# Kernel optimization log

Measured on AMD Instinct MI355X. Metric: run time of the kernel, lower is better.

## Reference

```python
import jax, jax.numpy as jnp
import numpy as np

N_USER, N_TX, E = 50000, 50000, 600000
D_USER, D_TX, D_ALIGN, HID, OUT = 128, 64, 128, 256, 128


def setup_inputs() -> dict:
    key = jax.random.key(0)
    ks = jax.random.split(key, 16)
    s = 0.05
    return {
        "x_user": jax.random.normal(ks[0], (N_USER, D_USER), jnp.float32),
        "x_tx": jax.random.normal(ks[1], (N_TX, D_TX), jnp.float32),
        "edge_user_tx": jax.random.randint(ks[2], (2, E), 0, N_USER),
        "edge_tx_user": jax.random.randint(ks[3], (2, E), 0, N_TX),
        "W_align_user": jax.random.normal(ks[4], (D_USER, D_ALIGN), jnp.float32) * s,
        "b_align_user": jnp.zeros((D_ALIGN,), jnp.float32),
        "W_align_tx": jax.random.normal(ks[5], (D_TX, D_ALIGN), jnp.float32) * s,
        "b_align_tx": jnp.zeros((D_ALIGN,), jnp.float32),
        "eps_ut": jnp.zeros((), jnp.float32),
        "eps_tu": jnp.zeros((), jnp.float32),
        "W1_ut": jax.random.normal(ks[6], (D_TX + D_ALIGN, HID), jnp.float32) * s,
        "b1_ut": jnp.zeros((HID,), jnp.float32),
        "W2_ut": jax.random.normal(ks[7], (HID, OUT), jnp.float32) * s,
        "b2_ut": jnp.zeros((OUT,), jnp.float32),
        "W1_tu": jax.random.normal(ks[8], (D_USER + D_ALIGN, HID), jnp.float32) * s,
        "b1_tu": jnp.zeros((HID,), jnp.float32),
        "W2_tu": jax.random.normal(ks[9], (HID, OUT), jnp.float32) * s,
        "b2_tu": jnp.zeros((OUT,), jnp.float32),
    }


def _mlp(h, W1, b1, W2, b2):
    return jnp.maximum(h @ W1 + b1, 0.0) @ W2 + b2


def _hexgin_conv(x_src, x_dst, edge_index, W_a, b_a, eps, W1, b1, W2, b2):
    # align src features, gather along edges, scatter-sum into dst nodes
    a_src = x_src @ W_a + b_a                       # [N_src, D_ALIGN]
    msgs = a_src[edge_index[0]]                     # [E, D_ALIGN] gather
    agg = jax.ops.segment_sum(msgs, edge_index[1], num_segments=x_dst.shape[0])
    h = jnp.concatenate([(1.0 + eps) * x_dst, agg], axis=1)
    return _mlp(h, W1, b1, W2, b2)


def reference(x_user, x_tx, edge_user_tx, edge_tx_user,
              W_align_user, b_align_user, W_align_tx, b_align_tx,
              eps_ut, eps_tu,
              W1_ut, b1_ut, W2_ut, b2_ut,
              W1_tu, b1_tu, W2_tu, b2_tu):
    # relation (user, makes, tx): updates tx nodes
    out_tx = _hexgin_conv(x_user, x_tx, edge_user_tx,
                          W_align_user, b_align_user, eps_ut,
                          W1_ut, b1_ut, W2_ut, b2_ut)
    # relation (tx, to, user): updates user nodes
    out_user = _hexgin_conv(x_tx, x_user, edge_tx_user,
                            W_align_tx, b_align_tx, eps_tu,
                            W1_tu, b1_tu, W2_tu, b2_tu)
    # HeteroConv aggr='sum': single relation per target, so plain outputs
    return out_user, out_tx
```

## Files before the change

kernel.cpp:

```cpp
#include <hip/hip_runtime.h>
#include <hip/hip_bf16.h>


#define D_USER 128
#define D_TX 64
#define D_ALIGN 128
#define HID 256
#define OUT_D 128
#define NNODE 50000
#define BI 32
#define MAXSLOT 62

typedef __attribute__((ext_vector_type(8))) short short8;
typedef __attribute__((ext_vector_type(4))) float f32x4;
typedef unsigned short ush;

__device__ __forceinline__ ush f2bf(float f) {
    union { float f; unsigned u; } v; v.f = f;
    unsigned u = v.u + 0x7fffu + ((v.u >> 16) & 1u);
    return (ush)(u >> 16);
}
__device__ __forceinline__ float2 bfu2f(unsigned u) {
    union { unsigned u; float f; } a, b;
    a.u = (u & 0xffffu) << 16;
    b.u = u & 0xffff0000u;
    return make_float2(a.f, b.f);
}
__device__ __forceinline__ unsigned f2bfu(float2 v) {
    return (unsigned)f2bf(v.x) | ((unsigned)f2bf(v.y) << 16);
}
__device__ __forceinline__ uint4 scale_bf8(uint4 v, float e) {
    unsigned* w = (unsigned*)&v;
    #pragma unroll
    for (int t = 0; t < 4; ++t) {
        float2 f = bfu2f(w[t]);
        w[t] = f2bfu(make_float2(f.x * e, f.y * e));
    }
    return v;
}

__global__ __launch_bounds__(256) void prep(
    const float* __restrict__ xu, ush* __restrict__ xbu,
    const float* __restrict__ xt, ush* __restrict__ xbt, int n8u, int n8t,
    const float* __restrict__ Wa_u, const float* __restrict__ ba_u,
    const float* __restrict__ W1_ut,
    const float* __restrict__ Wa_t, const float* __restrict__ ba_t,
    const float* __restrict__ W1_tu,
    const float* __restrict__ W2_ut, const float* __restrict__ W2_tu,
    ush* __restrict__ Bt1a, float* __restrict__ bfv1,
    ush* __restrict__ Bt1b, float* __restrict__ bfv2,
    ush* __restrict__ Bt2a, ush* __restrict__ Bt2b, int gb)
{
    int b = blockIdx.x, tid = threadIdx.x;
    if (b < gb) {
        int i = b * 256 + tid;
        const float* x; ush* xb; int j;
        if (i < n8u) { x = xu; xb = xbu; j = i; }
        else if (i < n8u + n8t) { x = xt; xb = xbt; j = i - n8u; }
        else return;
        const float4 a = *reinterpret_cast<const float4*>(&x[(size_t)j * 8]);
        const float4 c = *reinterpret_cast<const float4*>(&x[(size_t)j * 8 + 4]);
        ush o[8];
        o[0] = f2bf(a.x); o[1] = f2bf(a.y); o[2] = f2bf(a.z); o[3] = f2bf(a.w);
        o[4] = f2bf(c.x); o[5] = f2bf(c.y); o[6] = f2bf(c.z); o[7] = f2bf(c.w);
        *reinterpret_cast<uint4*>(&xb[(size_t)j * 8]) = *reinterpret_cast<uint4*>(o);
        return;
    }
    int idx = (b - gb) * 256 + tid;
    const int KT = 192;
    const int SEG1 = HID * (KT + 1);
    const int SEG2 = OUT_D * HID;
    if (idx < 2 * SEG1) {
        bool r2 = idx >= SEG1;
        int id = r2 ? idx - SEG1 : idx;
        const float* Wa = r2 ? Wa_t : Wa_u;
        const float* ba = r2 ? ba_t : ba_u;
        const float* W1 = r2 ? W1_tu : W1_ut;
        ush* Bt = r2 ? Bt1b : Bt1a;
        float* bfv = r2 ? bfv2 : bfv1;
        const int Dd = r2 ? 128 : 64;
        int c = id & (HID - 1);
        int k = id >> 8;
        const float* w1bot = W1 + (size_t)Dd * HID;
        if (k < Dd) {
            Bt[(size_t)c * KT + k] = f2bf(W1[(size_t)k * HID + c]);
        } else if (k < KT) {
            int ks = k - Dd;
            float acc = 0.f;
            for (int j = 0; j < D_ALIGN; ++j)
                acc += Wa[ks * D_ALIGN + j] * w1bot[(size_t)j * HID + c];
            Bt[(size_t)c * KT + k] = f2bf(acc);
        } else {
            float acc = 0.f;
            for (int j = 0; j < D_ALIGN; ++j)
                acc += ba[j] * w1bot[(size_t)j * HID + c];
            bfv[c] = acc;
        }
    } else if (idx < 2 * SEG1 + 2 * SEG2) {
        int id = idx - 2 * SEG1;
        bool r2 = id >= SEG2;
        if (r2) id -= SEG2;
        const float* W2 = r2 ? W2_tu : W2_ut;
        ush* Bt2 = r2 ? Bt2b : Bt2a;
        int c = id & (OUT_D - 1);
        int k = id >> 7;
        Bt2[(size_t)c * HID + k] = f2bf(W2[(size_t)k * OUT_D + c]);
    }
}

__global__ void fill_direct(const int* __restrict__ e_ut, const int* __restrict__ e_tu,
                            int E, int* __restrict__ pad)
{
    int i = blockIdx.x * blockDim.x + threadIdx.x;
    if (i >= 2 * E) return;
    int d, s;
    if (i < E) { d = e_ut[E + i];                    s = e_ut[i]; }
    else       { int j = i - E; d = NNODE + e_tu[E + j]; s = e_tu[j]; }
    int pos = atomicAdd(&pad[(size_t)d * BI], 1);
    if (pos < MAXSLOT)
        ((ush*)pad)[(size_t)d * (2 * BI) + 2 + pos] = (ush)s;
}

__device__ __forceinline__ int slot_word(const int* blk, int lane)
{
    return ((lane & 31) < 31) ? blk[1 + (lane & 31)] : 0;
}
__device__ __forceinline__ int slot_get(int word, int j)
{
    return (j & 1) ? ((word >> 16) & 0xffff) : (word & 0xffff);
}

__global__ __launch_bounds__(256) void agg_all(
    const ush* __restrict__ xbu, const ush* __restrict__ xbt,
    const int* __restrict__ pad, ush* __restrict__ Sb1, ush* __restrict__ Sb2)
{
    int w = (blockIdx.x * 256 + threadIdx.x) >> 6;
    if (w >= 2 * NNODE) return;
    const int lane = threadIdx.x & 63;
    const int* blk = pad + (size_t)w * BI;
    const int n = min(blk[0], MAXSLOT);
    const int word = slot_word(blk, lane);
    if (w < NNODE) {
        float2 acc = make_float2(0.f, 0.f);
        int i = 0;
        for (; i + 4 <= n; i += 4) {
            int wa = __shfl(word, i >> 1);
            int wb = __shfl(word, (i >> 1) + 1);
            int s0 = wa & 0xffff, s1 = (wa >> 16) & 0xffff;
            int s2 = wb & 0xffff, s3 = (wb >> 16) & 0xffff;
            unsigned v0 = *reinterpret_cast<const unsigned*>(&xbu[(size_t)s0 * 128 + 2 * lane]);
            unsigned v1 = *reinterpret_cast<const unsigned*>(&xbu[(size_t)s1 * 128 + 2 * lane]);
            unsigned v2 = *reinterpret_cast<const unsigned*>(&xbu[(size_t)s2 * 128 + 2 * lane]);
            unsigned v3 = *reinterpret_cast<const unsigned*>(&xbu[(size_t)s3 * 128 + 2 * lane]);
            float2 f0 = bfu2f(v0), f1 = bfu2f(v1), f2 = bfu2f(v2), f3 = bfu2f(v3);
            acc.x += (f0.x + f1.x) + (f2.x + f3.x);
            acc.y += (f0.y + f1.y) + (f2.y + f3.y);
        }
        for (; i < n; ++i) {
            int ww = __shfl(word, i >> 1);
            int s0 = slot_get(ww, i);
            unsigned v0 = *reinterpret_cast<const unsigned*>(&xbu[(size_t)s0 * 128 + 2 * lane]);
            float2 f0 = bfu2f(v0);
            acc.x += f0.x; acc.y += f0.y;
        }
        *reinterpret_cast<unsigned*>(&Sb1[(size_t)w * 128 + 2 * lane]) = f2bfu(acc);
    } else {
        const int w2 = w - NNODE;
        const int half = lane >> 5, l2 = lane & 31;
        float2 acc = make_float2(0.f, 0.f);
        int i = 0;
        for (; i + 4 <= n; i += 4) {
            int ja = i + half, jb = i + 2 + half;
            int wa = __shfl(word, ja >> 1);
            int wb = __shfl(word, jb >> 1);
            int s0 = slot_get(wa, ja), s1 = slot_get(wb, jb);
            unsigned v0 = *reinterpret_cast<const unsigned*>(&xbt[(size_t)s0 * 64 + 2 * l2]);
            unsigned v1 = *reinterpret_cast<const unsigned*>(&xbt[(size_t)s1 * 64 + 2 * l2]);
            float2 f0 = bfu2f(v0), f1 = bfu2f(v1);
            acc.x += f0.x + f1.x;
            acc.y += f0.y + f1.y;
        }
        for (; i + 2 <= n; i += 2) {
            int j = i + half;
            int ww = __shfl(word, j >> 1);
            int s0 = slot_get(ww, j);
            unsigned v0 = *reinterpret_cast<const unsigned*>(&xbt[(size_t)s0 * 64 + 2 * l2]);
            float2 f0 = bfu2f(v0);
            acc.x += f0.x; acc.y += f0.y;
        }
        if (i < n && half == 0) {
            int ww = __shfl(word, i >> 1);
            int s0 = slot_get(ww, i);
            unsigned v0 = *reinterpret_cast<const unsigned*>(&xbt[(size_t)s0 * 64 + 2 * l2]);
            float2 f0 = bfu2f(v0);
            acc.x += f0.x; acc.y += f0.y;
        }
        acc.x += __shfl_xor(acc.x, 32);
        acc.y += __shfl_xor(acc.y, 32);
        if (half == 0)
            *reinterpret_cast<unsigned*>(&Sb2[(size_t)w2 * 64 + 2 * l2]) = f2bfu(acc);
    }
}

__global__ __launch_bounds__(256) void mlp1_all(
    const ush* __restrict__ xbt, const ush* __restrict__ xbu,
    const ush* __restrict__ Sb1, const ush* __restrict__ Sb2,
    const ush* __restrict__ Bt1a, const ush* __restrict__ Bt1b,
    const float* __restrict__ bfv1, const float* __restrict__ bfv2,
    const float* __restrict__ b1_ut, const float* __restrict__ b1_tu,
    const int* __restrict__ pad,
    const float* __restrict__ eps_ut, const float* __restrict__ eps_tu,
    ush* __restrict__ hidb1, ush* __restrict__ hidb2, int M, int nb1)
{
    const int KT = 192;
    __shared__ ush As[128 * 40];
    __shared__ ush Bs[128 * 40];
    const int tid = threadIdx.x;
    const bool r2 = (int)blockIdx.y >= nb1;
    const int bm = (r2 ? blockIdx.y - nb1 : blockIdx.y) * 128;
    const int bn = blockIdx.x * 128;
    const ush* xdst = r2 ? xbu : xbt;
    const int Dd = r2 ? 128 : 64;
    const ush* Sb = r2 ? Sb2 : Sb1;
    const int Dsrc = r2 ? 64 : 128;
    const ush* Bt = r2 ? Bt1b : Bt1a;
    const float* bfv = r2 ? bfv2 : bfv1;
    const float* b1 = r2 ? b1_tu : b1_ut;
    const int* dgp = pad + (size_t)(r2 ? NNODE : 0) * BI;
    ush* hidb = r2 ? hidb2 : hidb1;
    const float e = 1.f + (r2 ? eps_tu[0] : eps_ut[0]);

    const int lane = tid & 63, wave = tid >> 6;
    const int wm = wave >> 1, wn = wave & 1;
    const int lo = lane & 15, hi = lane >> 4;

    f32x4 acc[4][4];
    #pragma unroll
    for (int m = 0; m < 4; ++m)
        #pragma unroll
        for (int n = 0; n < 4; ++n)
            acc[m][n] = f32x4{0.f, 0.f, 0.f, 0.f};

    for (int k0 = 0; k0 < KT; k0 += 32) {
        const ush* src = (k0 < Dd) ? xdst : Sb;
        const int ld   = (k0 < Dd) ? Dd : Dsrc;
        const int kb   = (k0 < Dd) ? k0 : k0 - Dd;
        const bool scale = (k0 < Dd);
        #pragma unroll
        for (int q = 0; q < 2; ++q) {
            int idx = tid + 256 * q;
            int r = idx >> 2, c8 = idx & 3;
            int gr = bm + r;
            uint4 v = uint4{0u, 0u, 0u, 0u};
            if (gr < M)
                v = *reinterpret_cast<const uint4*>(&src[(size_t)gr * ld + kb + c8 * 8]);
            if (scale) v = scale_bf8(v, e);
            *reinterpret_cast<uint4*>(&As[r * 40 + c8 * 8]) = v;
        }
        #pragma unroll
        for (int q = 0; q < 2; ++q) {
            int idx = tid + 256 * q;
            int c = idx >> 2, ku = idx & 3;
            uint4 v = *reinterpret_cast<const uint4*>(&Bt[(size_t)(bn + c) * KT + k0 + ku * 8]);
            *reinterpret_cast<uint4*>(&Bs[c * 40 + ku * 8]) = v;
        }
        __syncthreads();
        short8 av[4], bv[4];
        #pragma unroll
        for (int m = 0; m < 4; ++m)
            av[m] = *reinterpret_cast<const short8*>(&As[(wm * 64 + m * 16 + lo) * 40 + hi * 8]);
        #pragma unroll
        for (int n = 0; n < 4; ++n)
            bv[n] = *reinterpret_cast<const short8*>(&Bs[(wn * 64 + n * 16 + lo) * 40 + hi * 8]);
        #pragma unroll
        for (int m = 0; m < 4; ++m)
            #pragma unroll
            for (int n = 0; n < 4; ++n)
                acc[m][n] = __builtin_amdgcn_mfma_f32_16x16x32_bf16(av[m], bv[n], acc[m][n], 0, 0, 0);
        __syncthreads();
    }

    float b1v[4], bfl[4]; int gcv[4];
    #pragma unroll
    for (int n = 0; n < 4; ++n) {
        int gc = bn + wn * 64 + n * 16 + lo;
        gcv[n] = gc; b1v[n] = b1[gc]; bfl[n] = bfv[gc];
    }
    #pragma unroll
    for (int m = 0; m < 4; ++m)
        #pragma unroll
        for (int reg = 0; reg < 4; ++reg) {
            int gr = bm + wm * 64 + m * 16 + hi * 4 + reg;
            if (gr >= M) continue;
            float dgv = (float)dgp[(size_t)gr * BI];
            #pragma unroll
            for (int n = 0; n < 4; ++n) {
                float val = acc[m][n][reg] + b1v[n] + dgv * bfl[n];
                hidb[(size_t)gr * HID + gcv[n]] = f2bf(fmaxf(val, 0.f));
            }
        }
}

__global__ __launch_bounds__(256) void mlp2_all(
    const ush* __restrict__ hidb1, const ush* __restrict__ hidb2,
    const ush* __restrict__ Bt2a, const ush* __restrict__ Bt2b,
    const float* __restrict__ b2_ut, const float* __restrict__ b2_tu,
    float* __restrict__ out_tx, float* __restrict__ out_user, int M, int nb1)
{
    const int KT = 256;
    __shared__ ush As[128 * 40];
    __shared__ ush Bs[128 * 40];
    const int tid = threadIdx.x;
    const bool r2 = (int)blockIdx.y >= nb1;
    const int bm = (r2 ? blockIdx.y - nb1 : blockIdx.y) * 128;
    const ush* hidb = r2 ? hidb2 : hidb1;
    const ush* Bt2 = r2 ? Bt2b : Bt2a;
    const float* b2 = r2 ? b2_tu : b2_ut;
    float* out = r2 ? out_user : out_tx;

    const int lane = tid & 63, wave = tid >> 6;
    const int wm = wave >> 1, wn = wave & 1;
    const int lo = lane & 15, hi = lane >> 4;

    f32x4 acc[4][4];
    #pragma unroll
    for (int m = 0; m < 4; ++m)
        #pragma unroll
        for (int n = 0; n < 4; ++n)
            acc[m][n] = f32x4{0.f, 0.f, 0.f, 0.f};

    for (int k0 = 0; k0 < KT; k0 += 32) {
        #pragma unroll
        for (int q = 0; q < 2; ++q) {
            int idx = tid + 256 * q;
            int r = idx >> 2, ku = idx & 3;
            int gr = bm + r;
            uint4 v = uint4{0u, 0u, 0u, 0u};
            if (gr < M)
                v = *reinterpret_cast<const uint4*>(&hidb[(size_t)gr * KT + k0 + ku * 8]);
            *reinterpret_cast<uint4*>(&As[r * 40 + ku * 8]) = v;
        }
        #pragma unroll
        for (int q = 0; q < 2; ++q) {
            int idx = tid + 256 * q;
            int c = idx >> 2, ku = idx & 3;
            uint4 v = *reinterpret_cast<const uint4*>(&Bt2[(size_t)c * KT + k0 + ku * 8]);
            *reinterpret_cast<uint4*>(&Bs[c * 40 + ku * 8]) = v;
        }
        __syncthreads();
        short8 av[4], bv[4];
        #pragma unroll
        for (int m = 0; m < 4; ++m)
            av[m] = *reinterpret_cast<const short8*>(&As[(wm * 64 + m * 16 + lo) * 40 + hi * 8]);
        #pragma unroll
        for (int n = 0; n < 4; ++n)
            bv[n] = *reinterpret_cast<const short8*>(&Bs[(wn * 64 + n * 16 + lo) * 40 + hi * 8]);
        #pragma unroll
        for (int m = 0; m < 4; ++m)
            #pragma unroll
            for (int n = 0; n < 4; ++n)
                acc[m][n] = __builtin_amdgcn_mfma_f32_16x16x32_bf16(av[m], bv[n], acc[m][n], 0, 0, 0);
        __syncthreads();
    }

    float b2v[4]; int gcv[4];
    #pragma unroll
    for (int n = 0; n < 4; ++n) {
        int gc = wn * 64 + n * 16 + lo;
        gcv[n] = gc; b2v[n] = b2[gc];
    }
    #pragma unroll
    for (int m = 0; m < 4; ++m)
        #pragma unroll
        for (int reg = 0; reg < 4; ++reg) {
            int gr = bm + wm * 64 + m * 16 + hi * 4 + reg;
            if (gr >= M) continue;
            #pragma unroll
            for (int n = 0; n < 4; ++n)
                out[(size_t)gr * OUT_D + gcv[n]] = acc[m][n][reg] + b2v[n];
        }
}

extern "C" void kernel_launch(void* const* d_in, const int* in_sizes, int n_in,
                              void* d_out, int out_size, void* d_ws, size_t ws_size,
                              hipStream_t stream)
{
    const float* x_user   = (const float*)d_in[0];
    const float* x_tx     = (const float*)d_in[1];
    const int*   e_ut     = (const int*)d_in[2];
    const int*   e_tu     = (const int*)d_in[3];
    const float* Wa_user  = (const float*)d_in[4];
    const float* ba_user  = (const float*)d_in[5];
    const float* Wa_tx    = (const float*)d_in[6];
    const float* ba_tx    = (const float*)d_in[7];
    const float* eps_ut   = (const float*)d_in[8];
    const float* eps_tu   = (const float*)d_in[9];
    const float* W1_ut    = (const float*)d_in[10];
    const float* b1_ut    = (const float*)d_in[11];
    const float* W2_ut    = (const float*)d_in[12];
    const float* b2_ut    = (const float*)d_in[13];
    const float* W1_tu    = (const float*)d_in[14];
    const float* b1_tu    = (const float*)d_in[15];
    const float* W2_tu    = (const float*)d_in[16];
    const float* b2_tu    = (const float*)d_in[17];

    const int N_user = in_sizes[0] / D_USER;
    const int N_tx   = in_sizes[1] / D_TX;
    const int E      = in_sizes[2] / 2;
    const int NT     = 2 * NNODE;

    float* out_user = (float*)d_out;
    float* out_tx   = (float*)d_out + (size_t)N_user * OUT_D;

    int*   pad   = (int*)d_ws;
    float* fws   = (float*)d_ws;
    ush*   Bt1a  = (ush*)(fws + 3300000);
    ush*   Bt1b  = (ush*)(fws + 3330000);
    ush*   Bt2a  = (ush*)(fws + 3360000);
    ush*   Bt2b  = (ush*)(fws + 3380000);
    float* bfv1  = fws + 3400000;
    float* bfv2  = fws + 3401000;
    ush*   xbu   = (ush*)(fws + 3410000);
    ush*   xbt   = (ush*)(fws + 6700000);
    ush*   Sb1   = (ush*)(fws + 8400000);
    ush*   Sb2   = (ush*)(fws + 11700000);
    ush*   hidb1 = (ush*)(fws + 13400000);
    ush*   hidb2 = (ush*)(fws + 19900000);

    const int threads = 256;
    const int n8u = N_user * D_USER / 8, n8t = N_tx * D_TX / 8;
    const int gb  = (n8u + n8t + 255) / 256;
    const int gw  = (2 * HID * 193 + 2 * OUT_D * HID + 255) / 256;
    const int nb1 = (NNODE + 127) / 128;

    hipMemsetAsync(pad, 0, (size_t)NT * BI * sizeof(int), stream);
    prep<<<gb + gw, threads, 0, stream>>>(
        x_user, xbu, x_tx, xbt, n8u, n8t,
        Wa_user, ba_user, W1_ut, Wa_tx, ba_tx, W1_tu, W2_ut, W2_tu,
        Bt1a, bfv1, Bt1b, bfv2, Bt2a, Bt2b, gb);
    fill_direct<<<(2 * E + 255) / 256, threads, 0, stream>>>(e_ut, e_tu, E, pad);
    agg_all<<<(NT * 64 + 255) / 256, threads, 0, stream>>>(xbu, xbt, pad, Sb1, Sb2);
    dim3 g1(2, 2 * nb1);
    mlp1_all<<<g1, threads, 0, stream>>>(
        xbt, xbu, Sb1, Sb2, Bt1a, Bt1b, bfv1, bfv2, b1_ut, b1_tu,
        pad, eps_ut, eps_tu, hidb1, hidb2, NNODE, nb1);
    dim3 g2(1, 2 * nb1);
    mlp2_all<<<g2, threads, 0, stream>>>(
        hidb1, hidb2, Bt2a, Bt2b, b2_ut, b2_tu, out_tx, out_user, NNODE, nb1);
}
```

Baseline: 205.9 us.

## Split edge fill per relation and overlap it with prep and aggregation

Measured after the change: 199.6 us. 1.03x faster.

```diff
diff --git a/kernel.cpp b/kernel.cpp
--- a/kernel.cpp
+++ b/kernel.cpp
@@ -39,7 +39,18 @@
     return v;
 }
 
-__global__ __launch_bounds__(256) void prep(
+
+__device__ __forceinline__ void dev_fill(const int* __restrict__ e, int E, int i,
+                                         int* __restrict__ pad, int dbase)
+{
+    int d = dbase + e[E + i];
+    int s = e[i];
+    int pos = atomicAdd(&pad[(size_t)d * BI], 1);
+    if (pos < MAXSLOT)
+        ((ush*)pad)[(size_t)d * (2 * BI) + 2 + pos] = (ush)s;
+}
+
+__device__ __forceinline__ void dev_prep(int b, int tid,
     const float* __restrict__ xu, ush* __restrict__ xbu,
     const float* __restrict__ xt, ush* __restrict__ xbt, int n8u, int n8t,
     const float* __restrict__ Wa_u, const float* __restrict__ ba_u,
@@ -51,7 +62,6 @@
     ush* __restrict__ Bt1b, float* __restrict__ bfv2,
     ush* __restrict__ Bt2a, ush* __restrict__ Bt2b, int gb)
 {
-    int b = blockIdx.x, tid = threadIdx.x;
     if (b < gb) {
         int i = b * 256 + tid;
         const float* x; ush* xb; int j;
@@ -108,19 +118,6 @@
     }
 }
 
-__global__ void fill_direct(const int* __restrict__ e_ut, const int* __restrict__ e_tu,
-                            int E, int* __restrict__ pad)
-{
-    int i = blockIdx.x * blockDim.x + threadIdx.x;
-    if (i >= 2 * E) return;
-    int d, s;
-    if (i < E) { d = e_ut[E + i];                    s = e_ut[i]; }
-    else       { int j = i - E; d = NNODE + e_tu[E + j]; s = e_tu[j]; }
-    int pos = atomicAdd(&pad[(size_t)d * BI], 1);
-    if (pos < MAXSLOT)
-        ((ush*)pad)[(size_t)d * (2 * BI) + 2 + pos] = (ush)s;
-}
-
 __device__ __forceinline__ int slot_word(const int* blk, int lane)
 {
     return ((lane & 31) < 31) ? blk[1 + (lane & 31)] : 0;
@@ -130,76 +127,122 @@
     return (j & 1) ? ((word >> 16) & 0xffff) : (word & 0xffff);
 }
 
-__global__ __launch_bounds__(256) void agg_all(
-    const ush* __restrict__ xbu, const ush* __restrict__ xbt,
-    const int* __restrict__ pad, ush* __restrict__ Sb1, ush* __restrict__ Sb2)
-{
-    int w = (blockIdx.x * 256 + threadIdx.x) >> 6;
-    if (w >= 2 * NNODE) return;
-    const int lane = threadIdx.x & 63;
+__device__ __forceinline__ void dev_agg128(int w, int lane,
+    const ush* __restrict__ xbu, const int* __restrict__ pad, ush* __restrict__ Sb1)
+{
     const int* blk = pad + (size_t)w * BI;
     const int n = min(blk[0], MAXSLOT);
     const int word = slot_word(blk, lane);
-    if (w < NNODE) {
-        float2 acc = make_float2(0.f, 0.f);
-        int i = 0;
-        for (; i + 4 <= n; i += 4) {
-            int wa = __shfl(word, i >> 1);
-            int wb = __shfl(word, (i >> 1) + 1);
-            int s0 = wa & 0xffff, s1 = (wa >> 16) & 0xffff;
-            int s2 = wb & 0xffff, s3 = (wb >> 16) & 0xffff;
-            unsigned v0 = *reinterpret_cast<const unsigned*>(&xbu[(size_t)s0 * 128 + 2 * lane]);
-            unsigned v1 = *reinterpret_cast<const unsigned*>(&xbu[(size_t)s1 * 128 + 2 * lane]);
-            unsigned v2 = *reinterpret_cast<const unsigned*>(&xbu[(size_t)s2 * 128 + 2 * lane]);
-            unsigned v3 = *reinterpret_cast<const unsigned*>(&xbu[(size_t)s3 * 128 + 2 * lane]);
-            float2 f0 = bfu2f(v0), f1 = bfu2f(v1), f2 = bfu2f(v2), f3 = bfu2f(v3);
-            acc.x += (f0.x + f1.x) + (f2.x + f3.x);
-            acc.y += (f0.y + f1.y) + (f2.y + f3.y);
-        }
-        for (; i < n; ++i) {
-            int ww = __shfl(word, i >> 1);
-            int s0 = slot_get(ww, i);
-            unsigned v0 = *reinterpret_cast<const unsigned*>(&xbu[(size_t)s0 * 128 + 2 * lane]);
-            float2 f0 = bfu2f(v0);
-            acc.x += f0.x; acc.y += f0.y;
-        }
-        *reinterpret_cast<unsigned*>(&Sb1[(size_t)w * 128 + 2 * lane]) = f2bfu(acc);
+    float2 acc = make_float2(0.f, 0.f);
+    int i = 0;
+    for (; i + 4 <= n; i += 4) {
+        int wa = __shfl(word, i >> 1);
+        int wb = __shfl(word, (i >> 1) + 1);
+        int s0 = wa & 0xffff, s1 = (wa >> 16) & 0xffff;
+        int s2 = wb & 0xffff, s3 = (wb >> 16) & 0xffff;
+        unsigned v0 = *reinterpret_cast<const unsigned*>(&xbu[(size_t)s0 * 128 + 2 * lane]);
+        unsigned v1 = *reinterpret_cast<const unsigned*>(&xbu[(size_t)s1 * 128 + 2 * lane]);
+        unsigned v2 = *reinterpret_cast<const unsigned*>(&xbu[(size_t)s2 * 128 + 2 * lane]);
+        unsigned v3 = *reinterpret_cast<const unsigned*>(&xbu[(size_t)s3 * 128 + 2 * lane]);
+        float2 f0 = bfu2f(v0), f1 = bfu2f(v1), f2 = bfu2f(v2), f3 = bfu2f(v3);
+        acc.x += (f0.x + f1.x) + (f2.x + f3.x);
+        acc.y += (f0.y + f1.y) + (f2.y + f3.y);
+    }
+    for (; i < n; ++i) {
+        int ww = __shfl(word, i >> 1);
+        int s0 = slot_get(ww, i);
+        unsigned v0 = *reinterpret_cast<const unsigned*>(&xbu[(size_t)s0 * 128 + 2 * lane]);
+        float2 f0 = bfu2f(v0);
+        acc.x += f0.x; acc.y += f0.y;
+    }
+    *reinterpret_cast<unsigned*>(&Sb1[(size_t)w * 128 + 2 * lane]) = f2bfu(acc);
+}
+
+__device__ __forceinline__ void dev_agg64(int w2, int lane,
+    const ush* __restrict__ xbt, const int* __restrict__ pad, ush* __restrict__ Sb2)
+{
+    const int* blk = pad + (size_t)(NNODE + w2) * BI;
+    const int n = min(blk[0], MAXSLOT);
+    const int word = slot_word(blk, lane);
+    const int half = lane >> 5, l2 = lane & 31;
+    float2 acc = make_float2(0.f, 0.f);
+    int i = 0;
+    for (; i + 4 <= n; i += 4) {
+        int ja = i + half, jb = i + 2 + half;
+        int wa = __shfl(word, ja >> 1);
+        int wb = __shfl(word, jb >> 1);
+        int s0 = slot_get(wa, ja), s1 = slot_get(wb, jb);
+        unsigned v0 = *reinterpret_cast<const unsigned*>(&xbt[(size_t)s0 * 64 + 2 * l2]);
+        unsigned v1 = *reinterpret_cast<const unsigned*>(&xbt[(size_t)s1 * 64 + 2 * l2]);
+        float2 f0 = bfu2f(v0), f1 = bfu2f(v1);
+        acc.x += f0.x + f1.x;
+        acc.y += f0.y + f1.y;
+    }
+    for (; i + 2 <= n; i += 2) {
+        int j = i + half;
+        int ww = __shfl(word, j >> 1);
+        int s0 = slot_get(ww, j);
+        unsigned v0 = *reinterpret_cast<const unsigned*>(&xbt[(size_t)s0 * 64 + 2 * l2]);
+        float2 f0 = bfu2f(v0);
+        acc.x += f0.x; acc.y += f0.y;
+    }
+    if (i < n && half == 0) {
+        int ww = __shfl(word, i >> 1);
+        int s0 = slot_get(ww, i);
+        unsigned v0 = *reinterpret_cast<const unsigned*>(&xbt[(size_t)s0 * 64 + 2 * l2]);
+        float2 f0 = bfu2f(v0);
+        acc.x += f0.x; acc.y += f0.y;
+    }
+    acc.x += __shfl_xor(acc.x, 32);
+    acc.y += __shfl_xor(acc.y, 32);
+    if (half == 0)
+        *reinterpret_cast<unsigned*>(&Sb2[(size_t)w2 * 64 + 2 * l2]) = f2bfu(acc);
+}
+
+
+__global__ __launch_bounds__(256) void kA(
+    const int* __restrict__ e_ut, int E, int* __restrict__ pad,
+    const float* __restrict__ xu, ush* __restrict__ xbu,
+    const float* __restrict__ xt, ush* __restrict__ xbt, int n8u, int n8t,
+    const float* __restrict__ Wa_u, const float* __restrict__ ba_u,
+    const float* __restrict__ W1_ut,
+    const float* __restrict__ Wa_t, const float* __restrict__ ba_t,
+    const float* __restrict__ W1_tu,
+    const float* __restrict__ W2_ut, const float* __restrict__ W2_tu,
+    ush* __restrict__ Bt1a, float* __restrict__ bfv1,
+    ush* __restrict__ Bt1b, float* __restrict__ bfv2,
+    ush* __restrict__ Bt2a, ush* __restrict__ Bt2b, int gf, int gb)
+{
+    int b = blockIdx.x, tid = threadIdx.x;
+    if (b < gf) {
+        int i = b * 256 + tid;
+        if (i < E) dev_fill(e_ut, E, i, pad, 0);
     } else {
-        const int w2 = w - NNODE;
-        const int half = lane >> 5, l2 = lane & 31;
-        float2 acc = make_float2(0.f, 0.f);
-        int i = 0;
-        for (; i + 4 <= n; i += 4) {
-            int ja = i + half, jb = i + 2 + half;
-            int wa = __shfl(word, ja >> 1);
-            int wb = __shfl(word, jb >> 1);
-            int s0 = slot_get(wa, ja), s1 = slot_get(wb, jb);
-            unsigned v0 = *reinterpret_cast<const unsigned*>(&xbt[(size_t)s0 * 64 + 2 * l2]);
-            unsigned v1 = *reinterpret_cast<const unsigned*>(&xbt[(size_t)s1 * 64 + 2 * l2]);
-            float2 f0 = bfu2f(v0), f1 = bfu2f(v1);
-            acc.x += f0.x + f1.x;
-            acc.y += f0.y + f1.y;
-        }
-        for (; i + 2 <= n; i += 2) {
-            int j = i + half;
-            int ww = __shfl(word, j >> 1);
-            int s0 = slot_get(ww, j);
-            unsigned v0 = *reinterpret_cast<const unsigned*>(&xbt[(size_t)s0 * 64 + 2 * l2]);
-            float2 f0 = bfu2f(v0);
-            acc.x += f0.x; acc.y += f0.y;
-        }
-        if (i < n && half == 0) {
-            int ww = __shfl(word, i >> 1);
-            int s0 = slot_get(ww, i);
-            unsigned v0 = *reinterpret_cast<const unsigned*>(&xbt[(size_t)s0 * 64 + 2 * l2]);
-            float2 f0 = bfu2f(v0);
-            acc.x += f0.x; acc.y += f0.y;
-        }
-        acc.x += __shfl_xor(acc.x, 32);
-        acc.y += __shfl_xor(acc.y, 32);
-        if (half == 0)
-            *reinterpret_cast<unsigned*>(&Sb2[(size_t)w2 * 64 + 2 * l2]) = f2bfu(acc);
-    }
+        dev_prep(b - gf, tid, xu, xbu, xt, xbt, n8u, n8t,
+                 Wa_u, ba_u, W1_ut, Wa_t, ba_t, W1_tu, W2_ut, W2_tu,
+                 Bt1a, bfv1, Bt1b, bfv2, Bt2a, Bt2b, gb);
+    }
+}
+
+__global__ __launch_bounds__(256) void kB(
+    const int* __restrict__ e_tu, int E, int* __restrict__ pad,
+    const ush* __restrict__ xbu, ush* __restrict__ Sb1, int gf)
+{
+    int b = blockIdx.x, tid = threadIdx.x;
+    if (b < gf) {
+        int i = b * 256 + tid;
+        if (i < E) dev_fill(e_tu, E, i, pad, NNODE);
+    } else {
+        int w = (b - gf) * 4 + (tid >> 6);
+        if (w < NNODE) dev_agg128(w, tid & 63, xbu, pad, Sb1);
+    }
+}
+
+__global__ __launch_bounds__(256) void kC(
+    const ush* __restrict__ xbt, const int* __restrict__ pad, ush* __restrict__ Sb2)
+{
+    int w2 = blockIdx.x * 4 + (threadIdx.x >> 6);
+    if (w2 < NNODE) dev_agg64(w2, threadIdx.x & 63, xbt, pad, Sb2);
 }
 
 __global__ __launch_bounds__(256) void mlp1_all(
@@ -429,21 +472,28 @@
 
     const int threads = 256;
     const int n8u = N_user * D_USER / 8, n8t = N_tx * D_TX / 8;
+    const int gf  = (E + 255) / 256;
     const int gb  = (n8u + n8t + 255) / 256;
     const int gw  = (2 * HID * 193 + 2 * OUT_D * HID + 255) / 256;
+    const int ga  = (NNODE + 3) / 4;
     const int nb1 = (NNODE + 127) / 128;
 
     hipMemsetAsync(pad, 0, (size_t)NT * BI * sizeof(int), stream);
-    prep<<<gb + gw, threads, 0, stream>>>(
-        x_user, xbu, x_tx, xbt, n8u, n8t,
+
+    kA<<<gf + gb + gw, threads, 0, stream>>>(
+        e_ut, E, pad, x_user, xbu, x_tx, xbt, n8u, n8t,
         Wa_user, ba_user, W1_ut, Wa_tx, ba_tx, W1_tu, W2_ut, W2_tu,
-        Bt1a, bfv1, Bt1b, bfv2, Bt2a, Bt2b, gb);
-    fill_direct<<<(2 * E + 255) / 256, threads, 0, stream>>>(e_ut, e_tu, E, pad);
-    agg_all<<<(NT * 64 + 255) / 256, threads, 0, stream>>>(xbu, xbt, pad, Sb1, Sb2);
+        Bt1a, bfv1, Bt1b, bfv2, Bt2a, Bt2b, gf, gb);
+
+    kB<<<gf + ga, threads, 0, stream>>>(e_tu, E, pad, xbu, Sb1, gf);
+
+    kC<<<ga, threads, 0, stream>>>(xbt, pad, Sb2);
+
     dim3 g1(2, 2 * nb1);
     mlp1_all<<<g1, threads, 0, stream>>>(
         xbt, xbu, Sb1, Sb2, Bt1a, Bt1b, bfv1, bfv2, b1_ut, b1_tu,
         pad, eps_ut, eps_tu, hidb1, hidb2, NNODE, nb1);
+
     dim3 g2(1, 2 * nb1);
     mlp2_all<<<g2, threads, 0, stream>>>(
         hidb1, hidb2, Bt2a, Bt2b, b2_ut, b2_tu, out_tx, out_user, NNODE, nb1);
```
